# Kernel optimization log

Hardware: AMD Instinct MI355X
Metric: run time of the kernel (lower is better)

Reference implementation:

```python
import jax, jax.numpy as jnp
import numpy as np
from jax import lax

D_MODEL = 512
N_BLOCKS = 8
VOCAB = 2048
MEL = 80
D_INNER = 2 * D_MODEL      # standard Mamba expand=2
STATE = 16                 # AudioConstants.MAMBA_STATE_DIM
DT_RANK = D_MODEL // 16    # 32
CONV_K = 4                 # causal depthwise conv kernel
B, T = 4, 2048


def setup_inputs() -> dict:
    key = jax.random.key(0)
    ks = jax.random.split(key, 16)
    s = 0.02
    nb = N_BLOCKS
    inp = {
        "feats": jax.random.normal(ks[0], (B, T, MEL), jnp.float32),
        "feat_lens": jax.random.randint(ks[1], (B,), 0, T, jnp.int32),
        # frontend
        "conv1_w": jax.random.normal(ks[2], (D_MODEL, MEL, 3), jnp.float32) * s,
        "conv1_b": jnp.zeros((D_MODEL,), jnp.float32),
        "conv2_w": jax.random.normal(ks[3], (D_MODEL, D_MODEL, 3), jnp.float32) * s,
        "conv2_b": jnp.zeros((D_MODEL,), jnp.float32),
        # stacked per-block Mamba params (leading dim = n_blocks)
        "norm_w": jnp.ones((nb, D_MODEL), jnp.float32),
        "in_proj_w": jax.random.normal(ks[4], (nb, D_MODEL, 2 * D_INNER), jnp.float32) * s,
        "dwconv_w": jax.random.normal(ks[5], (nb, D_INNER, CONV_K), jnp.float32) * s,
        "dwconv_b": jnp.zeros((nb, D_INNER), jnp.float32),
        "x_proj_w": jax.random.normal(ks[6], (nb, D_INNER, DT_RANK + 2 * STATE), jnp.float32) * s,
        "dt_proj_w": jax.random.normal(ks[7], (nb, DT_RANK, D_INNER), jnp.float32) * s,
        "dt_proj_b": jnp.full((nb, D_INNER), -4.6, jnp.float32),  # softplus(-4.6)~0.01
        "A_log": jnp.tile(jnp.log(jnp.arange(1, STATE + 1, dtype=jnp.float32))[None, None, :], (nb, D_INNER, 1)),
        "Dskip": jnp.ones((nb, D_INNER), jnp.float32),
        "out_proj_w": jax.random.normal(ks[8], (nb, D_INNER, D_MODEL), jnp.float32) * s,
        # CTC head
        "head_w": jax.random.normal(ks[9], (D_MODEL, VOCAB), jnp.float32) * s,
        "head_b": jnp.zeros((VOCAB,), jnp.float32),
    }
    return inp


def _conv1d(x, w, b, stride, pad):
    # x: (B, Cin, L), w: (Cout, Cin, K)
    y = lax.conv_general_dilated(x, w, (stride,), [(pad, pad)],
                                 dimension_numbers=("NCH", "OIH", "NCH"))
    return y + b[None, :, None]


def _mamba_layer(x, p):
    nw, ipw, cw, cb, xpw, dpw, dpb, alog, dsk, opw = p
    res = x
    # RMSNorm
    xn = x * lax.rsqrt(jnp.mean(x * x, axis=-1, keepdims=True) + 1e-5) * nw
    xz = xn @ ipw                                # (B, L, 2*di)
    xs, z = jnp.split(xz, 2, axis=-1)
    # causal depthwise conv over time
    xc = jnp.pad(xs.transpose(0, 2, 1), ((0, 0), (0, 0), (CONV_K - 1, 0)))
    xc = lax.conv_general_dilated(xc, cw[:, None, :], (1,), [(0, 0)],
                                  dimension_numbers=("NCH", "OIH", "NCH"),
                                  feature_group_count=D_INNER)
    xs = jax.nn.silu((xc + cb[None, :, None]).transpose(0, 2, 1))  # (B, L, di)
    # input-dependent SSM params
    xdb = xs @ xpw                               # (B, L, dt_rank + 2N)
    dt, Bm, Cm = jnp.split(xdb, [DT_RANK, DT_RANK + STATE], axis=-1)
    delta = jax.nn.softplus(dt @ dpw + dpb)      # (B, L, di)
    A = -jnp.exp(alog)                           # (di, N)
    dA = jnp.exp(delta[..., None] * A)           # (B, L, di, N)
    dBx = delta[..., None] * Bm[:, :, None, :] * xs[..., None]

    def step(h, inp):
        dA_t, dBx_t, C_t = inp                   # (B,di,N),(B,di,N),(B,N)
        h = dA_t * h + dBx_t
        y = jnp.einsum("bdn,bn->bd", h, C_t)
        return h, y

    h0 = jnp.zeros((x.shape[0], D_INNER, STATE), x.dtype)
    _, ys = lax.scan(step, h0, (dA.transpose(1, 0, 2, 3),
                                dBx.transpose(1, 0, 2, 3),
                                Cm.transpose(1, 0, 2)))
    y = ys.transpose(1, 0, 2) + xs * dsk          # (B, L, di)
    y = y * jax.nn.silu(z)
    return res + y @ opw, None


def reference(feats, feat_lens, conv1_w, conv1_b, conv2_w, conv2_b,
              norm_w, in_proj_w, dwconv_w, dwconv_b, x_proj_w,
              dt_proj_w, dt_proj_b, A_log, Dskip, out_proj_w,
              head_w, head_b):
    x = feats.transpose(0, 2, 1)                  # (B, 80, T)
    x = jax.nn.gelu(_conv1d(x, conv1_w, conv1_b, 2, 1), approximate=False)
    x = jax.nn.gelu(_conv1d(x, conv2_w, conv2_b, 2, 1), approximate=False)
    x = x.transpose(0, 2, 1)                      # (B, T/4, D)
    params = (norm_w, in_proj_w, dwconv_w, dwconv_b, x_proj_w,
              dt_proj_w, dt_proj_b, A_log, Dskip, out_proj_w)
    x, _ = lax.scan(_mamba_layer, x, params)
    logits = x @ head_w + head_b                  # (B, T/4, V)
    out_lens = jnp.maximum(feat_lens // 4, 1)
    return logits, out_lens
```

## Files before the change

kernel.cpp:

```cpp
#include <hip/hip_runtime.h>
#include <hip/hip_bf16.h>

#define DMODEL 512
#define NB 8
#define VOCABSZ 2048
#define MEL 80
#define DIN 1024
#define NSTATE 16
#define BATCH 4
#define TIN 2048
#define LL1 1024
#define LSEQ 512
#define MROWS (BATCH*LSEQ)
#define M1ROWS (BATCH*LL1)
#define NCHUNK 32
#define LCHUNK 16

typedef unsigned short u16;
typedef unsigned int   u32;
typedef __attribute__((ext_vector_type(8))) short short8;
typedef __attribute__((ext_vector_type(4))) float f32x4;

__device__ __forceinline__ float bf2f(u16 v) { return __uint_as_float(((u32)v) << 16); }
__device__ __forceinline__ u16 f2bf(float f) {
    u32 u = __float_as_uint(f);
    return (u16)((u + 0x7fffu + ((u >> 16) & 1u)) >> 16);
}
__device__ __forceinline__ float gelu_exact(float v) {
    return 0.5f * v * (1.0f + erff(v * 0.70710678118654752f));
}
__device__ __forceinline__ float silu_f(float v) { return v / (1.0f + __expf(-v)); }
__device__ __forceinline__ float softplus_f(float v) { return v > 20.f ? v : log1pf(__expf(v)); }

template<int WM, int WN, int MR, int NR, int EPI, int SPLITK>
__global__ __launch_bounds__(WM*WN*64) void gemm2_bf16(
    const u16* __restrict__ A, int lda,
    const u16* __restrict__ BT, int ldb,
    const float* __restrict__ bias,
    float* __restrict__ Cf, u16* __restrict__ Cb, int ldc,
    int K, int zstride)
{
    constexpr int BM = WM * MR * 16;
    constexpr int BN = WN * NR * 16;
    constexpr int NT = WM * WN * 64;
    constexpr int LA = (BM * 4) / NT;
    constexpr int LB = (BN * 4) / NT;
    __shared__ __align__(16) u16 As[2][BM * 32];
    __shared__ __align__(16) u16 Bs[2][BN * 32];
    const int tid = threadIdx.x;
    const int m0 = blockIdx.y * BM, n0 = blockIdx.x * BN;
    const int lane = tid & 63;
    const int wave = tid >> 6;
    const int wm = wave / WN, wn = wave % WN;
    const int lr = lane & 15, lk = lane >> 4;

    int kt0 = 0, kend = K;
    if (SPLITK > 1) {
        const int kb = K / SPLITK;
        kt0 = blockIdx.z * kb;
        kend = kt0 + kb;
        Cf += (size_t)blockIdx.z * zstride;
    }

    f32x4 acc[MR][NR];
#pragma unroll
    for (int m = 0; m < MR; ++m)
#pragma unroll
        for (int n = 0; n < NR; ++n) acc[m][n] = (f32x4){0.f, 0.f, 0.f, 0.f};

    auto stage = [&](int buf, int kt) {
#pragma unroll
        for (int c = 0; c < LA; ++c) {
            int idx = c * NT + tid;
            const u16* src = A + (size_t)(m0 + (idx >> 2)) * lda + kt + (idx & 3) * 8;
            __builtin_amdgcn_global_load_lds(
                (const __attribute__((address_space(1))) void*)src,
                (__attribute__((address_space(3))) void*)&As[buf][idx * 8], 16, 0, 0);
        }
#pragma unroll
        for (int c = 0; c < LB; ++c) {
            int idx = c * NT + tid;
            const u16* src = BT + (size_t)(n0 + (idx >> 2)) * ldb + kt + (idx & 3) * 8;
            __builtin_amdgcn_global_load_lds(
                (const __attribute__((address_space(1))) void*)src,
                (__attribute__((address_space(3))) void*)&Bs[buf][idx * 8], 16, 0, 0);
        }
    };

    stage(0, kt0);
    __syncthreads();
    int cur = 0;
    for (int kt = kt0; kt < kend; kt += 32) {
        if (kt + 32 < kend) stage(cur ^ 1, kt + 32);
        short8 a[MR], b[NR];
#pragma unroll
        for (int m = 0; m < MR; ++m)
            a[m] = *(const short8*)&As[cur][((wm * MR + m) * 16 + lr) * 32 + lk * 8];
#pragma unroll
        for (int n = 0; n < NR; ++n)
            b[n] = *(const short8*)&Bs[cur][((wn * NR + n) * 16 + lr) * 32 + lk * 8];
#pragma unroll
        for (int m = 0; m < MR; ++m)
#pragma unroll
            for (int n = 0; n < NR; ++n)
                acc[m][n] = __builtin_amdgcn_mfma_f32_16x16x32_bf16(a[m], b[n], acc[m][n], 0, 0, 0);
        __syncthreads();
        cur ^= 1;
    }

#pragma unroll
    for (int m = 0; m < MR; ++m) {
#pragma unroll
        for (int n = 0; n < NR; ++n) {
#pragma unroll
            for (int r = 0; r < 4; ++r) {
                const int row = m0 + (wm * MR + m) * 16 + lk * 4 + r;
                const int col = n0 + (wn * NR + n) * 16 + lr;
                float v = acc[m][n][r];
                if (EPI == 1)      v += bias[col];
                else if (EPI == 2) v = gelu_exact(v + bias[col]);
                else if (EPI == 3) v = softplus_f(v + bias[col]);
                else if (EPI == 4) v += Cf[(size_t)row * ldc + col];
                else if (EPI == 6) v *= bias[row];
                if (Cf) Cf[(size_t)row * ldc + col] = v;
                if (Cb) Cb[(size_t)row * ldc + col] = f2bf(v);
            }
        }
    }
}

__global__ __launch_bounds__(256) void tcast_k(const float* __restrict__ in, u16* __restrict__ out,
                                               int R, int C, size_t sin, size_t sout) {
    in  += (size_t)blockIdx.z * sin;
    out += (size_t)blockIdx.z * sout;
    __shared__ float s[32][33];
    const int tx = threadIdx.x & 31, ty = threadIdx.x >> 5;
    const int r0 = blockIdx.y * 32, c0 = blockIdx.x * 32;
#pragma unroll
    for (int i = 0; i < 4; ++i)
        s[ty + i * 8][tx] = in[(size_t)(r0 + ty + i * 8) * C + c0 + tx];
    __syncthreads();
#pragma unroll
    for (int i = 0; i < 4; ++i)
        out[(size_t)(c0 + ty + i * 8) * R + r0 + tx] = f2bf(s[tx][ty + i * 8]);
}

__global__ __launch_bounds__(256) void tcast_nw_k(const float* __restrict__ in, u16* __restrict__ out,
                                                  const float* __restrict__ nwp,
                                                  int R, int C, size_t sin, size_t sout, int nws) {
    in  += (size_t)blockIdx.z * sin;
    out += (size_t)blockIdx.z * sout;
    nwp += (size_t)blockIdx.z * nws;
    __shared__ float s[32][33];
    const int tx = threadIdx.x & 31, ty = threadIdx.x >> 5;
    const int r0 = blockIdx.y * 32, c0 = blockIdx.x * 32;
#pragma unroll
    for (int i = 0; i < 4; ++i)
        s[ty + i * 8][tx] = in[(size_t)(r0 + ty + i * 8) * C + c0 + tx];
    __syncthreads();
    const float nwv = nwp[r0 + tx];
#pragma unroll
    for (int i = 0; i < 4; ++i)
        out[(size_t)(c0 + ty + i * 8) * R + r0 + tx] = f2bf(s[tx][ty + i * 8] * nwv);
}

__global__ void castpad_k(const float* __restrict__ in, u16* __restrict__ out,
                          int rows, int cin, int cout, int instride,
                          size_t sin, size_t sout) {
    in  += (size_t)blockIdx.z * sin;
    out += (size_t)blockIdx.z * sout;
    int idx = blockIdx.x * 256 + threadIdx.x;
    if (idx >= rows * cout) return;
    int c = idx % cout, r = idx / cout;
    out[idx] = (c < cin) ? f2bf(in[(size_t)r * instride + c]) : (u16)0;
}

__global__ void im2col1_k(const float* __restrict__ feats, u16* __restrict__ out,
                          const int* __restrict__ feat_lens, float* __restrict__ lens_out) {
    int idx = blockIdx.x * 256 + threadIdx.x;
    if (blockIdx.x == 0 && threadIdx.x < BATCH) {
        int v = feat_lens[threadIdx.x] / 4;
        if (v < 1) v = 1;
        lens_out[threadIdx.x] = (float)v;
    }
    int c = idx & 255, m = idx >> 8;
    int l1 = m & (LL1 - 1), b = m >> 10;
    float v = 0.f;
    if (c < 240) {
        int ci = c / 3, kk = c - ci * 3;
        int t = 2 * l1 - 1 + kk;
        if (t >= 0 && t < TIN) v = feats[((size_t)b * TIN + t) * MEL + ci];
    }
    out[idx] = f2bf(v);
}

__global__ void im2col2_k(const u16* __restrict__ y1b, u16* __restrict__ out) {
    int idx = blockIdx.x * 256 + threadIdx.x;
    int c = idx % 1536, m = idx / 1536;
    int l = m & (LSEQ - 1), b = m >> 9;
    int ci = c / 3, kk = c - ci * 3;
    int t = 2 * l - 1 + kk;
    out[idx] = (t >= 0 && t < LL1) ? y1b[((size_t)b * LL1 + t) * 512 + ci] : (u16)0;
}

__global__ __launch_bounds__(256) void rowsc_k(const float* __restrict__ X,
                                               float* __restrict__ scrow) {
    const int lane = threadIdx.x & 63;
    const int row = blockIdx.x * 4 + (threadIdx.x >> 6);
    const float4 v0 = *(const float4*)&X[(size_t)row * 512 + lane * 8];
    const float4 v1 = *(const float4*)&X[(size_t)row * 512 + lane * 8 + 4];
    float ss = v0.x * v0.x + v0.y * v0.y + v0.z * v0.z + v0.w * v0.w
             + v1.x * v1.x + v1.y * v1.y + v1.z * v1.z + v1.w * v1.w;
#pragma unroll
    for (int o = 1; o < 64; o <<= 1) ss += __shfl_xor(ss, o);
    if (lane == 0) scrow[row] = rsqrtf(ss * (1.f / 512.f) + 1e-5f);
}

__global__ __launch_bounds__(256) void dwconv_silu_k(const u16* __restrict__ xzb,
                                                     const float* __restrict__ cw,
                                                     const float* __restrict__ cb,
                                                     u16* __restrict__ xsb) {
    int d = blockIdx.x * 256 + threadIdx.x;
    int m = blockIdx.y;
    int l = m & (LSEQ - 1);
    int b = m >> 9;
    float acc = cb[d];
    const float4 w4 = *reinterpret_cast<const float4*>(&cw[d * 4]);
    const float wk[4] = {w4.x, w4.y, w4.z, w4.w};
#pragma unroll
    for (int k = 0; k < 4; k++) {
        int t = l - 3 + k;
        if (t >= 0) acc += wk[k] * bf2f(xzb[((size_t)(b * LSEQ + t)) * (2 * DIN) + d]);
    }
    xsb[(size_t)m * DIN + d] = f2bf(silu_f(acc));
}

__global__ void xreduce_k(const float* __restrict__ part, float* __restrict__ xdb,
                          u16* __restrict__ dtb) {
    int i4 = blockIdx.x * 256 + threadIdx.x;
    const float4 p0 = *(const float4*)&part[i4 * 4];
    const float4 p1 = *(const float4*)&part[131072 + i4 * 4];
    const float4 p2 = *(const float4*)&part[262144 + i4 * 4];
    const float4 p3 = *(const float4*)&part[393216 + i4 * 4];
    float4 s;
    s.x = p0.x + p1.x + p2.x + p3.x;
    s.y = p0.y + p1.y + p2.y + p3.y;
    s.z = p0.z + p1.z + p2.z + p3.z;
    s.w = p0.w + p1.w + p2.w + p3.w;
    *(float4*)&xdb[i4 * 4] = s;
    int c4 = i4 & 15, r = i4 >> 4;
    if (c4 < 8) {
        u32 lo = (u32)f2bf(s.x) | ((u32)f2bf(s.y) << 16);
        u32 hi = (u32)f2bf(s.z) | ((u32)f2bf(s.w) << 16);
        *(u32*)&dtb[r * 32 + c4 * 4]     = lo;
        *(u32*)&dtb[r * 32 + c4 * 4 + 2] = hi;
    }
}

template<int PASS>
__global__ __launch_bounds__(256) void scan_chunk_k(
    const u16* __restrict__ deltab, const u16* __restrict__ xsb,
    const float* __restrict__ xdb, const u16* __restrict__ xzb,
    const float* __restrict__ alog, const float* __restrict__ dsk,
    float* __restrict__ P, float* __restrict__ Q,
    u16* __restrict__ yb)
{
    __shared__ float s_bc[LCHUNK * 32];
    __shared__ float s_dl[LCHUNK * 64];
    __shared__ float s_xs[LCHUNK * 64];
    __shared__ float s_z [PASS ? LCHUNK * 64 : 1];

    const int tid  = threadIdx.x;
    const int j    = tid & 3;
    const int dsub = tid >> 2;
    const int d0   = blockIdx.x * 64;
    const int c    = blockIdx.y;
    const int b    = blockIdx.z;
    const int d    = d0 + dsub;
    const size_t rbase = (size_t)b * LSEQ + c * LCHUNK;

    for (int idx = tid; idx < LCHUNK * 32; idx += 256) {
        int t = idx >> 5, cc = idx & 31;
        s_bc[idx] = xdb[(rbase + t) * 64 + 32 + cc];
    }
    for (int idx = tid; idx < LCHUNK * 64; idx += 256) {
        int t = idx >> 6, dd = idx & 63;
        s_dl[idx] = bf2f(deltab[(rbase + t) * DIN + d0 + dd]);
        s_xs[idx] = bf2f(xsb[(rbase + t) * DIN + d0 + dd]);
        if (PASS) s_z[idx] = bf2f(xzb[(rbase + t) * (2 * DIN) + DIN + d0 + dd]);
    }
    __syncthreads();

    float a[4], h[4];
#pragma unroll
    for (int nj = 0; nj < 4; nj++)
        a[nj] = -__expf(alog[(size_t)d * NSTATE + j * 4 + nj]);

    const size_t chstride = (size_t)DIN * NSTATE;
    const size_t chcol = (size_t)d * NSTATE + j * 4;
    h[0] = h[1] = h[2] = h[3] = 0.f;
    if (PASS) {
        for (int c2 = 0; c2 < c; ++c2) {
            const size_t o = ((size_t)(b * NCHUNK + c2)) * chstride + chcol;
            const float4 Pv = *(const float4*)&P[o];
            const float4 Qv = *(const float4*)&Q[o];
            h[0] = fmaf(Pv.x, h[0], Qv.x);
            h[1] = fmaf(Pv.y, h[1], Qv.y);
            h[2] = fmaf(Pv.z, h[2], Qv.z);
            h[3] = fmaf(Pv.w, h[3], Qv.w);
        }
    }
    const float dskv = PASS ? dsk[d] : 0.f;
    float sdl = 0.f;

    for (int t = 0; t < LCHUNK; t++) {
        const float dl = s_dl[t * 64 + dsub];
        const float xv = s_xs[t * 64 + dsub];
        const float dlx = dl * xv;
        if (!PASS) sdl += dl;
        float yv = 0.f;
#pragma unroll
        for (int nj = 0; nj < 4; nj++) {
            const float bn = s_bc[t * 32 + j * 4 + nj];
            const float dA = __expf(dl * a[nj]);
            h[nj] = fmaf(dA, h[nj], dlx * bn);
            if (PASS) {
                const float cn = s_bc[t * 32 + 16 + j * 4 + nj];
                yv = fmaf(h[nj], cn, yv);
            }
        }
        if (PASS) {
            yv += __shfl_xor(yv, 1);
            yv += __shfl_xor(yv, 2);
            if (j == 0) {
                const float zv = s_z[t * 64 + dsub];
                yb[(rbase + t) * DIN + d] = f2bf((yv + xv * dskv) * silu_f(zv));
            }
        }
    }

    if (!PASS) {
        const size_t o = ((size_t)(b * NCHUNK + c)) * chstride + chcol;
        float4 Pv, Qv;
        Pv.x = __expf(a[0] * sdl); Pv.y = __expf(a[1] * sdl);
        Pv.z = __expf(a[2] * sdl); Pv.w = __expf(a[3] * sdl);
        Qv.x = h[0]; Qv.y = h[1]; Qv.z = h[2]; Qv.w = h[3];
        *(float4*)&P[o] = Pv;
        *(float4*)&Q[o] = Qv;
    }
}

extern "C" void kernel_launch(void* const* d_in, const int* in_sizes, int n_in,
                              void* d_out, int out_size, void* d_ws, size_t ws_size,
                              hipStream_t stream)
{
    const float* feats = (const float*)d_in[0];
    const int*   flens = (const int*)  d_in[1];
    const float* c1w = (const float*)d_in[2];
    const float* c1b = (const float*)d_in[3];
    const float* c2w = (const float*)d_in[4];
    const float* c2b = (const float*)d_in[5];
    const float* nw  = (const float*)d_in[6];
    const float* ipw = (const float*)d_in[7];
    const float* cw  = (const float*)d_in[8];
    const float* cb  = (const float*)d_in[9];
    const float* xpw = (const float*)d_in[10];
    const float* dpw = (const float*)d_in[11];
    const float* dpb = (const float*)d_in[12];
    const float* alog= (const float*)d_in[13];
    const float* dskp= (const float*)d_in[14];
    const float* opw = (const float*)d_in[15];
    const float* hw  = (const float*)d_in[16];
    const float* hb  = (const float*)d_in[17];

    float* ws = (float*)d_ws;
    u16*  XZb    = (u16*)ws;
    float* X     = ws + 2097152;
    u16*  Xb     = (u16*)(ws + 3145728);
    float* scrow = ws + 3670016;
    u16*  XSb    = (u16*)(ws + 4194304);
    u16*  DELb   = (u16*)(ws + 5242880);
    float* XDB   = ws + 6291456;
    u16*  dtb    = (u16*)(ws + 6422528);
    float* P     = ws + 6455296;
    u16*  Yb     = (u16*)(ws + 8552448);
    float* XDBp  = ws + 9601024;
    u16*  ipwTa  = (u16*)(ws + 10125312);
    u16*  opwTa  = (u16*)(ws + 14319616);
    u16*  hwT    = (u16*)(ws + 16416768);
    u16*  xpwT   = (u16*)(ws + 16941056);
    u16*  dpwT   = (u16*)(ws + 17203200);
    u16*  c1wb   = (u16*)(ws + 17334272);
    u16*  c2wb   = (u16*)(ws + 17399808);
    u16*  Y1b    = XSb;
    float* logits = (float*)d_out;
    float* Q     = logits;

    castpad_k<<<dim3(512, 1, 1), 256, 0, stream>>>(c1w, c1wb, 512, 240, 256, 240, 0, 0);
    castpad_k<<<dim3(3072, 1, 1), 256, 0, stream>>>(c2w, c2wb, 512, 1536, 1536, 1536, 0, 0);
    tcast_k<<<dim3(64, 16, 1), 256, 0, stream>>>(hw, hwT, 512, 2048, 0, 0);
    tcast_k<<<dim3(2, 32, 8), 256, 0, stream>>>(xpw, xpwT, 1024, 64, 65536, 65536);
    tcast_k<<<dim3(32, 1, 8), 256, 0, stream>>>(dpw, dpwT, 32, 1024, 32768, 32768);
    tcast_nw_k<<<dim3(64, 16, 8), 256, 0, stream>>>(ipw, ipwTa, nw, 512, 2048,
                                                    1048576, 1048576, DMODEL);
    tcast_k<<<dim3(16, 32, 8), 256, 0, stream>>>(opw, opwTa, 1024, 512, 524288, 524288);

    im2col1_k<<<4096, 256, 0, stream>>>(feats, XZb, flens, logits + (size_t)MROWS * VOCABSZ);
    gemm2_bf16<2, 2, 4, 2, 2, 1><<<dim3(8, 32), 256, 0, stream>>>(
        XZb, 256, c1wb, 256, c1b, nullptr, Y1b, 512, 256, 0);
    im2col2_k<<<12288, 256, 0, stream>>>(Y1b, XZb);
    gemm2_bf16<2, 2, 2, 2, 2, 1><<<dim3(8, 32), 256, 0, stream>>>(
        XZb, 1536, c2wb, 1536, c2b, X, Xb, 512, 1536, 0);

    for (int blk = 0; blk < NB; ++blk) {
        rowsc_k<<<512, 256, 0, stream>>>(X, scrow);
        gemm2_bf16<2, 2, 4, 2, 6, 1><<<dim3(32, 16), 256, 0, stream>>>(
            Xb, 512, ipwTa + (size_t)blk * 1048576, 512, scrow,
            nullptr, XZb, 2048, 512, 0);
        dwconv_silu_k<<<dim3(4, MROWS), 256, 0, stream>>>(
            XZb, cw + blk * DIN * 4, cb + blk * DIN, XSb);
        gemm2_bf16<2, 2, 2, 2, 0, 4><<<dim3(1, 32, 4), 256, 0, stream>>>(
            XSb, 1024, xpwT + (size_t)blk * 65536, 1024, nullptr,
            XDBp, nullptr, 64, 1024, 131072);
        xreduce_k<<<128, 256, 0, stream>>>(XDBp, XDB, dtb);
        gemm2_bf16<2, 2, 4, 2, 3, 1><<<dim3(16, 16), 256, 0, stream>>>(
            dtb, 32, dpwT + (size_t)blk * 32768, 32, dpb + blk * DIN,
            nullptr, DELb, 1024, 32, 0);
        scan_chunk_k<0><<<dim3(16, NCHUNK, BATCH), 256, 0, stream>>>(
            DELb, XSb, XDB, nullptr, alog + (size_t)blk * DIN * NSTATE,
            nullptr, P, Q, nullptr);
        scan_chunk_k<1><<<dim3(16, NCHUNK, BATCH), 256, 0, stream>>>(
            DELb, XSb, XDB, XZb, alog + (size_t)blk * DIN * NSTATE,
            dskp + blk * DIN, P, Q, Yb);
        gemm2_bf16<2, 2, 2, 2, 4, 1><<<dim3(8, 32), 256, 0, stream>>>(
            Yb, 1024, opwTa + (size_t)blk * 524288, 1024, nullptr,
            X, Xb, 512, 1024, 0);
    }

    gemm2_bf16<2, 2, 4, 2, 1, 1><<<dim3(32, 16), 256, 0, stream>>>(
        Xb, 512, hwT, 512, hb, logits, nullptr, 2048, 512, 0);
}
```

Before: 885.1 us.

## Fuse split-K reduction into dt projection and scan, enlarge scan chunks

Removes the separate xreduce kernel. The dt_proj GEMM now sums the four split-K partials directly into bf16 LDS tiles and runs a single-K-step MFMA with a softplus epilogue. The scan kernels sum the B/C partials on load instead of reading a reduced buffer. The scan chunking also changes from 32 chunks of 16 to 16 chunks of 32, which halves the grid of the scan kernels and lengthens each sequential chunk. Each scan block now re-reads the four partial buffers, which adds some redundant traffic.

Result: faster. 863.6 us (-2.4%).

```diff
diff --git a/kernel.cpp b/kernel.cpp
--- a/kernel.cpp
+++ b/kernel.cpp
@@ -13,8 +13,8 @@
 #define LSEQ 512
 #define MROWS (BATCH*LSEQ)
 #define M1ROWS (BATCH*LL1)
-#define NCHUNK 32
-#define LCHUNK 16
+#define NCHUNK 16
+#define LCHUNK 32
 
 typedef unsigned short u16;
 typedef unsigned int   u32;
@@ -235,32 +235,71 @@
     xsb[(size_t)m * DIN + d] = f2bf(silu_f(acc));
 }
 
-__global__ void xreduce_k(const float* __restrict__ part, float* __restrict__ xdb,
-                          u16* __restrict__ dtb) {
-    int i4 = blockIdx.x * 256 + threadIdx.x;
-    const float4 p0 = *(const float4*)&part[i4 * 4];
-    const float4 p1 = *(const float4*)&part[131072 + i4 * 4];
-    const float4 p2 = *(const float4*)&part[262144 + i4 * 4];
-    const float4 p3 = *(const float4*)&part[393216 + i4 * 4];
-    float4 s;
-    s.x = p0.x + p1.x + p2.x + p3.x;
-    s.y = p0.y + p1.y + p2.y + p3.y;
-    s.z = p0.z + p1.z + p2.z + p3.z;
-    s.w = p0.w + p1.w + p2.w + p3.w;
-    *(float4*)&xdb[i4 * 4] = s;
-    int c4 = i4 & 15, r = i4 >> 4;
-    if (c4 < 8) {
-        u32 lo = (u32)f2bf(s.x) | ((u32)f2bf(s.y) << 16);
-        u32 hi = (u32)f2bf(s.z) | ((u32)f2bf(s.w) << 16);
-        *(u32*)&dtb[r * 32 + c4 * 4]     = lo;
-        *(u32*)&dtb[r * 32 + c4 * 4 + 2] = hi;
+__global__ __launch_bounds__(256) void dtproj_k(
+    const float* __restrict__ part, const u16* __restrict__ dpwT,
+    const float* __restrict__ dpb, u16* __restrict__ delb)
+{
+    __shared__ __align__(16) u16 As[128 * 32];
+    __shared__ __align__(16) u16 Bs[64 * 32];
+    const int tid = threadIdx.x;
+    const int m0 = blockIdx.y * 128, n0 = blockIdx.x * 64;
+    {
+        const int r = tid >> 1, hh = (tid & 1) * 16;
+        const size_t o = (size_t)(m0 + r) * 64 + hh;
+        float4 s[4];
+#pragma unroll
+        for (int q = 0; q < 4; ++q) {
+            s[q] = *(const float4*)&part[o + q * 4];
+#pragma unroll
+            for (int p = 1; p < 4; ++p) {
+                const float4 v = *(const float4*)&part[(size_t)p * 131072 + o + q * 4];
+                s[q].x += v.x; s[q].y += v.y; s[q].z += v.z; s[q].w += v.w;
+            }
+        }
+        u32 pk[8];
+#pragma unroll
+        for (int q = 0; q < 4; ++q) {
+            pk[2 * q]     = (u32)f2bf(s[q].x) | ((u32)f2bf(s[q].y) << 16);
+            pk[2 * q + 1] = (u32)f2bf(s[q].z) | ((u32)f2bf(s[q].w) << 16);
+        }
+        *(uint4*)&As[r * 32 + hh]     = make_uint4(pk[0], pk[1], pk[2], pk[3]);
+        *(uint4*)&As[r * 32 + hh + 8] = make_uint4(pk[4], pk[5], pk[6], pk[7]);
+    }
+    {
+        const int row = tid >> 2, p4 = (tid & 3) * 8;
+        const u16* src = dpwT + (size_t)(n0 + row) * 32 + p4;
+        __builtin_amdgcn_global_load_lds(
+            (const __attribute__((address_space(1))) void*)src,
+            (__attribute__((address_space(3))) void*)&Bs[row * 32 + p4], 16, 0, 0);
+    }
+    __syncthreads();
+    const int lane = tid & 63, wave = tid >> 6;
+    const int wm = wave >> 1, wn = wave & 1;
+    const int lr = lane & 15, lk = lane >> 4;
+    short8 b8[2];
+#pragma unroll
+    for (int n = 0; n < 2; ++n)
+        b8[n] = *(const short8*)&Bs[((wn * 2 + n) * 16 + lr) * 32 + lk * 8];
+#pragma unroll
+    for (int m = 0; m < 4; ++m) {
+        const short8 a8 = *(const short8*)&As[((wm * 4 + m) * 16 + lr) * 32 + lk * 8];
+#pragma unroll
+        for (int n = 0; n < 2; ++n) {
+            f32x4 acc = __builtin_amdgcn_mfma_f32_16x16x32_bf16(a8, b8[n], (f32x4){0.f,0.f,0.f,0.f}, 0, 0, 0);
+#pragma unroll
+            for (int r = 0; r < 4; ++r) {
+                const int row = m0 + (wm * 4 + m) * 16 + lk * 4 + r;
+                const int col = n0 + (wn * 2 + n) * 16 + lr;
+                delb[(size_t)row * DIN + col] = f2bf(softplus_f(acc[r] + dpb[col]));
+            }
+        }
     }
 }
 
 template<int PASS>
 __global__ __launch_bounds__(256) void scan_chunk_k(
     const u16* __restrict__ deltab, const u16* __restrict__ xsb,
-    const float* __restrict__ xdb, const u16* __restrict__ xzb,
+    const float* __restrict__ part, const u16* __restrict__ xzb,
     const float* __restrict__ alog, const float* __restrict__ dsk,
     float* __restrict__ P, float* __restrict__ Q,
     u16* __restrict__ yb)
@@ -281,7 +320,8 @@
 
     for (int idx = tid; idx < LCHUNK * 32; idx += 256) {
         int t = idx >> 5, cc = idx & 31;
-        s_bc[idx] = xdb[(rbase + t) * 64 + 32 + cc];
+        const size_t o = (rbase + t) * 64 + 32 + cc;
+        s_bc[idx] = part[o] + part[131072 + o] + part[262144 + o] + part[393216 + o];
     }
     for (int idx = tid; idx < LCHUNK * 64; idx += 256) {
         int t = idx >> 6, dd = idx & 63;
@@ -380,11 +420,9 @@
     float* scrow = ws + 3670016;
     u16*  XSb    = (u16*)(ws + 4194304);
     u16*  DELb   = (u16*)(ws + 5242880);
-    float* XDB   = ws + 6291456;
-    u16*  dtb    = (u16*)(ws + 6422528);
-    float* P     = ws + 6455296;
-    u16*  Yb     = (u16*)(ws + 8552448);
-    float* XDBp  = ws + 9601024;
+    float* P     = ws + 6291456;
+    u16*  Yb     = (u16*)(ws + 7340032);
+    float* XDBp  = ws + 8388608;
     u16*  ipwTa  = (u16*)(ws + 10125312);
     u16*  opwTa  = (u16*)(ws + 14319616);
     u16*  hwT    = (u16*)(ws + 16416768);
@@ -422,15 +460,13 @@
         gemm2_bf16<2, 2, 2, 2, 0, 4><<<dim3(1, 32, 4), 256, 0, stream>>>(
             XSb, 1024, xpwT + (size_t)blk * 65536, 1024, nullptr,
             XDBp, nullptr, 64, 1024, 131072);
-        xreduce_k<<<128, 256, 0, stream>>>(XDBp, XDB, dtb);
-        gemm2_bf16<2, 2, 4, 2, 3, 1><<<dim3(16, 16), 256, 0, stream>>>(
-            dtb, 32, dpwT + (size_t)blk * 32768, 32, dpb + blk * DIN,
-            nullptr, DELb, 1024, 32, 0);
+        dtproj_k<<<dim3(16, 16), 256, 0, stream>>>(
+            XDBp, dpwT + (size_t)blk * 32768, dpb + blk * DIN, DELb);
         scan_chunk_k<0><<<dim3(16, NCHUNK, BATCH), 256, 0, stream>>>(
-            DELb, XSb, XDB, nullptr, alog + (size_t)blk * DIN * NSTATE,
+            DELb, XSb, XDBp, nullptr, alog + (size_t)blk * DIN * NSTATE,
             nullptr, P, Q, nullptr);
         scan_chunk_k<1><<<dim3(16, NCHUNK, BATCH), 256, 0, stream>>>(
-            DELb, XSb, XDB, XZb, alog + (size_t)blk * DIN * NSTATE,
+            DELb, XSb, XDBp, XZb, alog + (size_t)blk * DIN * NSTATE,
             dskp + blk * DIN, P, Q, Yb);
         gemm2_bf16<2, 2, 2, 2, 4, 1><<<dim3(8, 32), 256, 0, stream>>>(
             Yb, 1024, opwTa + (size_t)blk * 524288, 1024, nullptr,
```
